# Kernel tuning notes

Measured on AMD Instinct MI355X. Metric: run time of the kernel, lower is better.

## Reference

```python
import jax, jax.numpy as jnp
import numpy as np

N, NF, DIM, H, DH, DEPTH, EDIM, NB = 256, 127, 128, 8, 64, 6, 3, 512
INNER = H * DH  # 512
SCALE = DH ** -0.5
EPS = 1e-5


def setup_inputs() -> dict:
    key = jax.random.key(0)
    ks = jax.random.split(key, 16)
    p = lambda k, shape: jax.random.normal(k, shape, jnp.float32) * 0.02
    return {
        "coordinates": jax.random.normal(ks[0], (N, 3), jnp.float32),
        "bonds": jax.random.randint(ks[1], (NB, 2), 0, N),
        "noise_level": jax.random.uniform(ks[2], (1,), jnp.float32),
        "atom_emb": p(ks[3], (N, NF)),
        "ln1_g": jnp.ones((DEPTH, DIM)), "ln1_b": jnp.zeros((DEPTH, DIM)),
        "Wq": p(ks[4], (DEPTH, DIM, INNER)), "bq": jnp.zeros((DEPTH, INNER)),
        "Wkv": p(ks[5], (DEPTH, DIM, 2 * INNER)), "bkv": jnp.zeros((DEPTH, 2 * INNER)),
        "We": p(ks[6], (DEPTH, EDIM, INNER)), "be": jnp.zeros((DEPTH, INNER)),
        "Wo": p(ks[7], (DEPTH, INNER, DIM)), "bo": jnp.zeros((DEPTH, DIM)),
        "Wg1": p(ks[8], (DEPTH, 3 * DIM)),
        "ln2_g": jnp.ones((DEPTH, DIM)), "ln2_b": jnp.zeros((DEPTH, DIM)),
        "W1": p(ks[9], (DEPTH, DIM, 4 * DIM)), "b1": jnp.zeros((DEPTH, 4 * DIM)),
        "W2": p(ks[10], (DEPTH, 4 * DIM, DIM)), "b2": jnp.zeros((DEPTH, DIM)),
        "Wg2": p(ks[11], (DEPTH, 3 * DIM)),
        "out_w": p(ks[12], (DIM, 1)), "out_b": jnp.zeros((1,)),
    }


def _layernorm(x, g, b):
    m = jnp.mean(x, axis=-1, keepdims=True)
    v = jnp.mean((x - m) ** 2, axis=-1, keepdims=True)
    return (x - m) * jax.lax.rsqrt(v + EPS) * g + b


def _gated_residual(x, res, Wg):
    # Linear(3*dim -> 1, no bias) then sigmoid; mask is all-True so no masking.
    gate = jax.nn.sigmoid(jnp.concatenate([x, res, x - res], axis=-1) @ Wg)[..., None]
    return x * gate + res * (1.0 - gate)


def _forward(coordinates, bonds, noise_level, atom_emb, ln1_g, ln1_b, Wq, bq,
             Wkv, bkv, We, be, Wo, bo, Wg1, ln2_g, ln2_b, W1, b1, W2, b2, Wg2,
             out_w, out_b):
    n = coordinates.shape[0]
    # nodes: [n, NF] atom embeddings (looked up at arange(n)) + noise column -> [n, DIM]
    noise_col = jnp.broadcast_to(noise_level.reshape(1, 1), (n, 1))
    nodes = jnp.concatenate([atom_emb, noise_col], axis=-1)
    # dense edge tensor [n, n, 3]: coordinate differences at bonded pairs, antisymmetric
    bi, bj = bonds[:, 0], bonds[:, 1]
    diff = coordinates[bi] - coordinates[bj]
    edges = jnp.zeros((n, n, EDIM), jnp.float32).at[bi, bj].set(diff).at[bj, bi].set(-diff)

    for l in range(DEPTH):
        # --- edge-biased multi-head attention (PreNorm) ---
        x = _layernorm(nodes, ln1_g[l], ln1_b[l])
        q = (x @ Wq[l] + bq[l]).reshape(n, H, DH).transpose(1, 0, 2)          # [h, i, d]
        kv = x @ Wkv[l] + bkv[l]
        k = kv[:, :INNER].reshape(n, H, DH).transpose(1, 0, 2)                # [h, j, d]
        v = kv[:, INNER:].reshape(n, H, DH).transpose(1, 0, 2)                # [h, j, d]
        e = (edges @ We[l] + be[l]).reshape(n, n, H, DH).transpose(2, 0, 1, 3)  # [h, i, j, d]
        k_ij = k[:, None, :, :] + e                                            # [h, i, j, d]
        v_ij = v[:, None, :, :] + e
        sim = jnp.einsum('hid,hijd->hij', q, k_ij) * SCALE
        attn = jax.nn.softmax(sim, axis=-1)  # mask is all ones -> no-op
        out = jnp.einsum('hij,hijd->hid', attn, v_ij)                          # [h, i, d]
        out = out.transpose(1, 0, 2).reshape(n, INNER) @ Wo[l] + bo[l]         # [n, DIM]
        nodes = _gated_residual(out, nodes, Wg1[l])
        # --- feedforward (PreNorm) + gated residual ---
        y = _layernorm(nodes, ln2_g[l], ln2_b[l])
        y = jax.nn.gelu(y @ W1[l] + b1[l], approximate=False) @ W2[l] + b2[l]
        nodes = _gated_residual(y, nodes, Wg2[l])

    energy = nodes @ out_w + out_b  # [n, 1]
    return energy[None, :, :]       # [1, n, 1]


def reference(coordinates, bonds, noise_level, atom_emb, ln1_g, ln1_b, Wq, bq,
              Wkv, bkv, We, be, Wo, bo, Wg1, ln2_g, ln2_b, W1, b1, W2, b2, Wg2,
              out_w, out_b):
    return _forward(coordinates, bonds, noise_level, atom_emb, ln1_g, ln1_b,
                    Wq, bq, Wkv, bkv, We, be, Wo, bo, Wg1, ln2_g, ln2_b,
                    W1, b1, W2, b2, Wg2, out_w, out_b)
```

## Files before the change

kernel.cpp:

```cpp
#include <hip/hip_runtime.h>

#define NN     256
#define NF     127
#define DIM    128
#define NH     8
#define DH     64
#define INNER  512
#define DEPTH  6
#define NB     512
#define ATTN_SCALE 0.125f
#define LN_EPS 1e-5f

typedef _Float16 f16;
union H8 { uint4 u; f16 h[8]; };

#define FMA4(A_, S_, V_) { A_.x=fmaf(S_,(V_).x,A_.x); A_.y=fmaf(S_,(V_).y,A_.y); \
                           A_.z=fmaf(S_,(V_).z,A_.z); A_.w=fmaf(S_,(V_).w,A_.w); }

__device__ __forceinline__ float wred_sum(float v){
#pragma unroll
  for(int o=32;o;o>>=1) v += __shfl_xor(v,o);
  return v;
}
__device__ __forceinline__ float wred_max(float v){
#pragma unroll
  for(int o=32;o;o>>=1) v = fmaxf(v,__shfl_xor(v,o));
  return v;
}
__device__ __forceinline__ float2 wred_sum2(float a, float b){
#pragma unroll
  for(int o=32;o;o>>=1){ a += __shfl_xor(a,o); b += __shfl_xor(b,o); }
  return make_float2(a,b);
}

__device__ __forceinline__ void ln_wave(float n0, float n1,
                                        const float* g, const float* b, int l,
                                        float& x0, float& x1){
  float2 sv = wred_sum2(n0+n1, n0*n0+n1*n1);
  float m  = sv.x*(1.f/DIM);
  float var = sv.y*(1.f/DIM) - m*m;
  float rs = rsqrtf(var + LN_EPS);
  x0 = (n0-m)*rs*g[l]    + b[l];
  x1 = (n1-m)*rs*g[64+l] + b[64+l];
}

__device__ __forceinline__ void gate_wave(float o0, float o1, float& n0, float& n1,
                                          const float* Wg, int l){
  float gv = o0*Wg[l]    + n0*Wg[DIM+l]    + (o0-n0)*Wg[2*DIM+l]
           + o1*Wg[64+l] + n1*Wg[DIM+64+l] + (o1-n1)*Wg[2*DIM+64+l];
  gv = wred_sum(gv);
  float gate = 1.f/(1.f + expf(-gv));
  n0 = o0*gate + n0*(1.f-gate);
  n1 = o1*gate + n1*(1.f-gate);
}

__device__ __forceinline__ void mvp128_512h(const float* __restrict__ xin,
                                            const f16* __restrict__ W,
                                            float* __restrict__ SC, int t){
  const int cg8 = (t&63)<<3, fg = t>>6, f0 = fg<<4;
  const f16* __restrict__ p = W + f0*INNER + cg8;
  float4 a0 = make_float4(0.f,0.f,0.f,0.f), a1 = a0;
#pragma unroll
  for(int k=0;k<16;k++){
    H8 wv; wv.u = *(const uint4*)(p + k*INNER);
    float x = xin[f0+k];
    a0.x=fmaf(x,(float)wv.h[0],a0.x); a0.y=fmaf(x,(float)wv.h[1],a0.y);
    a0.z=fmaf(x,(float)wv.h[2],a0.z); a0.w=fmaf(x,(float)wv.h[3],a0.w);
    a1.x=fmaf(x,(float)wv.h[4],a1.x); a1.y=fmaf(x,(float)wv.h[5],a1.y);
    a1.z=fmaf(x,(float)wv.h[6],a1.z); a1.w=fmaf(x,(float)wv.h[7],a1.w);
  }
  *(float4*)(SC + fg*INNER + cg8)     = a0;
  *(float4*)(SC + fg*INNER + cg8 + 4) = a1;
}
__device__ __forceinline__ void mvp512_128h(const float* __restrict__ ain,
                                            const f16* __restrict__ W,
                                            float* __restrict__ SC, int t){
  const int cg8 = (t&15)<<3, fg = t>>4, f0 = fg<<4;
  const f16* __restrict__ p = W + f0*DIM + cg8;
  float4 a0 = make_float4(0.f,0.f,0.f,0.f), a1 = a0;
#pragma unroll
  for(int k=0;k<16;k++){
    H8 wv; wv.u = *(const uint4*)(p + k*DIM);
    float x = ain[f0+k];
    a0.x=fmaf(x,(float)wv.h[0],a0.x); a0.y=fmaf(x,(float)wv.h[1],a0.y);
    a0.z=fmaf(x,(float)wv.h[2],a0.z); a0.w=fmaf(x,(float)wv.h[3],a0.w);
    a1.x=fmaf(x,(float)wv.h[4],a1.x); a1.y=fmaf(x,(float)wv.h[5],a1.y);
    a1.z=fmaf(x,(float)wv.h[6],a1.z); a1.w=fmaf(x,(float)wv.h[7],a1.w);
  }
  *(float4*)(SC + fg*DIM + cg8)     = a0;
  *(float4*)(SC + fg*DIM + cg8 + 4) = a1;
}
__device__ __forceinline__ void mvp128_1024(const float* __restrict__ xin,
                                            const float* __restrict__ W,
                                            float* __restrict__ SC, int t){
  const int cg4 = (t&255)<<2, rh = t>>8;
  float4 acc = make_float4(0.f,0.f,0.f,0.f);
#pragma unroll 8
  for(int f=rh*64; f<rh*64+64; f++){
    float4 wv = *(const float4*)(W + f*(2*INNER) + cg4);
    float xv = xin[f];
    FMA4(acc, xv, wv);
  }
  *(float4*)(SC + rh*(2*INNER) + cg4) = acc;
}

__device__ __forceinline__ void qkv_tail(const float* __restrict__ xs, int i,
    const f16* __restrict__ Wqh, const float* __restrict__ bq,
    const float* __restrict__ Wkv, const float* __restrict__ bkv,
    const float* __restrict__ be, float* qgn, float* kTn, float* vgn,
    float* __restrict__ SC, int t){
  mvp128_512h(xs, Wqh, SC,        t);
  mvp128_1024(xs, Wkv, SC + 4096, t);
  __syncthreads();
  {
    float s = bq[t];
#pragma unroll
    for(int fg=0; fg<8; fg++) s += SC[fg*INNER + t];
    qgn[i*INNER + t] = s;
  }
#pragma unroll
  for(int cc=0; cc<2; cc++){
    int c = t + cc*512;
    float sv = bkv[c] + SC[4096 + c] + SC[4096 + 1024 + c];
    if(c < INNER) kTn[c*NN + i]            = sv + be[c];
    else          vgn[i*INNER + c - INNER] = sv + be[c-INNER];
  }
}

__global__ __launch_bounds__(512) void k_prep(
    const float* __restrict__ Wq, const float* __restrict__ Wo,
    const float* __restrict__ W1, const float* __restrict__ W2,
    f16* Wqh, f16* Woh, f16* W1h, f16* W2h)
{
  const int NQ = DEPTH*DIM*INNER;
  const int NTOT = 4*NQ;
  for(int k = blockIdx.x*512 + threadIdx.x; k < NTOT; k += gridDim.x*512){
    float v; f16* dst;
    if(k < NQ)        { v = Wq[k];        dst = Wqh + k; }
    else if(k < 2*NQ) { v = Wo[k-NQ];     dst = Woh + (k-NQ); }
    else if(k < 3*NQ) { v = W1[k-2*NQ];   dst = W1h + (k-2*NQ); }
    else              { v = W2[k-3*NQ];   dst = W2h + (k-3*NQ); }
    *dst = (f16)v;
  }
}

__global__ __launch_bounds__(512) void k_qkv0(const float* atom_emb, const float* noise,
    float* nodes, const float* ln1_g, const float* ln1_b,
    const f16* Wqh, const float* bq, const float* Wkv, const float* bkv, const float* be,
    float* qg, float* kT, float* vg,
    const int* bonds, const float* coords, float* ebg){
  __shared__ __align__(16) float SC[6144];
  __shared__ __align__(16) float xsm[DIM];
  __shared__ __align__(16) float ebs[8*768];
  const int t = threadIdx.x, bid = blockIdx.x;
  if(bid >= NN){
    const int i0 = (bid-NN)<<3;
#pragma unroll
    for(int cc=0; cc<12; cc++) ebs[cc*512 + t] = 0.f;
    __syncthreads();
    {
      const int bi = bonds[2*t], bj = bonds[2*t+1];
      const bool hi = (bi>=i0 && bi<i0+8), hj = (bj>=i0 && bj<i0+8);
      if(hi || hj){
        float dx = coords[3*bi+0] - coords[3*bj+0];
        float dy = coords[3*bi+1] - coords[3*bj+1];
        float dz = coords[3*bi+2] - coords[3*bj+2];
        if(hi){ float* e = ebs + (bi-i0)*768; e[bj]=dx;  e[256+bj]=dy;  e[512+bj]=dz;  }
        if(hj){ float* e = ebs + (bj-i0)*768; e[bi]=-dx; e[256+bi]=-dy; e[512+bi]=-dz; }
      }
    }
    __syncthreads();
#pragma unroll
    for(int cc=0; cc<12; cc++) ebg[(size_t)i0*768 + cc*512 + t] = ebs[cc*512 + t];
    return;
  }
  const int i = bid, w = t>>6, l = t&63;
  float nd0 = (l<NF)?    atom_emb[i*NF + l]      : noise[0];
  float nd1 = (64+l<NF)? atom_emb[i*NF + 64 + l] : noise[0];
  if(w==0){ nodes[i*DIM + l] = nd0; nodes[i*DIM + 64 + l] = nd1; }
  float x0, x1;
  ln_wave(nd0, nd1, ln1_g, ln1_b, l, x0, x1);
  xsm[l] = x0; xsm[64+l] = x1;
  __syncthreads();
  qkv_tail(xsm, i, Wqh, bq, Wkv, bkv, be, qg, kT, vg, SC, t);
}

__global__ __launch_bounds__(512) void k_attn(
    const float* __restrict__ qg, const float* __restrict__ kT,
    const float* __restrict__ vg, const float* __restrict__ ebg,
    const float* __restrict__ We, float* __restrict__ aog,
    const f16* __restrict__ pfA, const f16* __restrict__ pfB,
    const f16* __restrict__ pfC, const f16* __restrict__ pfD,
    const float* __restrict__ pfE, int pf_next)
{
  __shared__ __align__(16) float kTs[64*NN];
  __shared__ __align__(16) float vs[NN*64];
  __shared__ __align__(16) float aW[8][NN];
  __shared__ __align__(16) float qsm[8*DH];
  const int t = threadIdx.x;
  const int h = blockIdx.x >> 5, i0 = (blockIdx.x & 31) << 3;
  const int w = t>>6, l = t&63;
  const int qb = h*DH, j0 = l<<2;

  {
    const float* kbase = kT + qb*NN;
#pragma unroll
    for(int r=0;r<8;r++){
      int idx = r*2048 + (t<<2);
      *(float4*)(kTs + idx) = *(const float4*)(kbase + idx);
    }
    const int jr = t>>4, c4 = (t&15)<<2;
#pragma unroll
    for(int p=0;p<8;p++){
      int j = p*32 + jr;
      *(float4*)(vs + j*64 + c4) = *(const float4*)(vg + j*INNER + qb + c4);
    }
  }
  qsm[w*DH + l] = qg[(i0+w)*INNER + qb + l];

  {
    const int s = blockIdx.x >> 3;
    unsigned keep = 0u;
    if(t < 256){
      keep ^= ((const uint4*)((const char*)pfA + (size_t)s*4096))[t].x;
      keep ^= ((const uint4*)((const char*)pfB + (size_t)s*4096))[t].y;
      keep ^= ((const uint4*)((const char*)pfC + (size_t)s*4096))[t].z;
      if(pf_next)
        keep ^= ((const uint4*)((const char*)pfD + (size_t)s*4096))[t].w;
    }
    if(pf_next){
      keep ^= ((const uint4*)((const char*)pfE + (size_t)s*16384))[t].x;
      keep ^= ((const uint4*)((const char*)pfE + (size_t)s*16384))[512 + t].x;
    }
    asm volatile("" :: "v"(keep));
  }
  __syncthreads();

  float qwe0, qwe1, qwe2;
  {
    float qv = qsm[w*DH + l];
    qwe0 = qv*We[0*INNER + qb + l];
    qwe1 = qv*We[1*INNER + qb + l];
    qwe2 = qv*We[2*INNER + qb + l];
#pragma unroll
    for(int o=32;o;o>>=1){
      qwe0 += __shfl_xor(qwe0,o); qwe1 += __shfl_xor(qwe1,o); qwe2 += __shfl_xor(qwe2,o);
    }
  }
  float s0=0.f,s1=0.f,s2=0.f,s3=0.f;
#pragma unroll 8
  for(int o=0;o<DH;o++){
    float qv = qsm[w*DH + o];
    float4 kk = *(const float4*)(kTs + o*NN + j0);
    s0=fmaf(qv,kk.x,s0); s1=fmaf(qv,kk.y,s1); s2=fmaf(qv,kk.z,s2); s3=fmaf(qv,kk.w,s3);
  }
  const float* __restrict__ e = ebg + (size_t)(i0+w)*768;
  float4 ex = *(const float4*)(e + j0);
  float4 ey = *(const float4*)(e + 256 + j0);
  float4 ez = *(const float4*)(e + 512 + j0);
  s0 = (s0 + qwe0*ex.x + qwe1*ey.x + qwe2*ez.x)*ATTN_SCALE;
  s1 = (s1 + qwe0*ex.y + qwe1*ey.y + qwe2*ez.y)*ATTN_SCALE;
  s2 = (s2 + qwe0*ex.z + qwe1*ey.z + qwe2*ez.z)*ATTN_SCALE;
  s3 = (s3 + qwe0*ex.w + qwe1*ey.w + qwe2*ez.w)*ATTN_SCALE;
  float mx = wred_max(fmaxf(fmaxf(s0,s1),fmaxf(s2,s3)));
  float p0=expf(s0-mx), p1=expf(s1-mx), p2=expf(s2-mx), p3=expf(s3-mx);
  float inv = 1.f / wred_sum(p0+p1+p2+p3);
  float a0=p0*inv, a1=p1*inv, a2=p2*inv, a3=p3*inv;
  *(float4*)(aW[w] + j0) = make_float4(a0,a1,a2,a3);
  float c0 = a0*ex.x + a1*ex.y + a2*ex.z + a3*ex.w;
  float c1 = a0*ey.x + a1*ey.y + a2*ey.z + a3*ey.w;
  float c2 = a0*ez.x + a1*ez.y + a2*ez.z + a3*ez.w;
  c0 = wred_sum(c0); c1 = wred_sum(c1); c2 = wred_sum(c2);
  __builtin_amdgcn_wave_barrier();
  const float* aww = aW[w];
  float acc0 = 0.f, acc1 = 0.f;
#pragma unroll 8
  for(int j=0;j<NN;j+=2){
    acc0 = fmaf(aww[j],   vs[j*64 + l],     acc0);
    acc1 = fmaf(aww[j+1], vs[(j+1)*64 + l], acc1);
  }
  float ov = acc0 + acc1
           + c0*We[0*INNER + qb + l]
           + c1*We[1*INNER + qb + l]
           + c2*We[2*INNER + qb + l];
  aog[(i0+w)*INNER + qb + l] = ov;
}

__global__ __launch_bounds__(512) void k_layer(
    float* nodes, const float* __restrict__ aog,
    float* qg_n, float* kT_n, float* vg_n,
    const f16* __restrict__ Woh, const float* __restrict__ bo,
    const float* __restrict__ Wg1,
    const float* __restrict__ ln2_g, const float* __restrict__ ln2_b,
    const f16* __restrict__ W1h, const float* __restrict__ b1,
    const f16* __restrict__ W2h, const float* __restrict__ b2,
    const float* __restrict__ Wg2,
    const float* __restrict__ ln1_g_n, const float* __restrict__ ln1_b_n,
    const f16* __restrict__ Wqh_n, const float* __restrict__ bq_n,
    const float* __restrict__ Wkv_n, const float* __restrict__ bkv_n,
    const float* __restrict__ be_n,
    const float* __restrict__ out_w, const float* __restrict__ out_b,
    float* eout, int has_next)
{
  __shared__ __align__(16) float SC[6144];
  __shared__ __align__(16) float qs[INNER];
  __shared__ __align__(16) float aos[INNER];
  __shared__ __align__(16) float xsm[DIM];
  const int t = threadIdx.x, i = blockIdx.x;
  const int w = t>>6, l = t&63;

  aos[t] = aog[i*INNER + t];
  float nd0 = nodes[i*DIM + l];
  float nd1 = nodes[i*DIM + 64 + l];
  __syncthreads();

  mvp512_128h(aos, Woh, SC, t);
  __syncthreads();
  {
    float o0 = bo[l], o1 = bo[64+l];
#pragma unroll
    for(int fg=0; fg<32; fg++){ o0 += SC[fg*DIM + l]; o1 += SC[fg*DIM + 64 + l]; }
    gate_wave(o0, o1, nd0, nd1, Wg1, l);
    float x0, x1;
    ln_wave(nd0, nd1, ln2_g, ln2_b, l, x0, x1);
    xsm[l] = x0; xsm[64+l] = x1;
  }
  __syncthreads();

  mvp128_512h(xsm, W1h, SC, t);
  __syncthreads();
  {
    float a = b1[t];
#pragma unroll
    for(int fg=0; fg<8; fg++) a += SC[fg*INNER + t];
    qs[t] = 0.5f*a*(1.f + erff(a*0.70710678118654752440f));
  }
  __syncthreads();
  mvp512_128h(qs, W2h, SC, t);
  __syncthreads();
  {
    float y0 = b2[l], y1 = b2[64+l];
#pragma unroll
    for(int fg=0; fg<32; fg++){ y0 += SC[fg*DIM + l]; y1 += SC[fg*DIM + 64 + l]; }
    gate_wave(y0, y1, nd0, nd1, Wg2, l);
    if(w==0){ nodes[i*DIM + l] = nd0; nodes[i*DIM + 64 + l] = nd1; }
    if(has_next){
      float x0, x1;
      ln_wave(nd0, nd1, ln1_g_n, ln1_b_n, l, x0, x1);
      xsm[l] = x0; xsm[64+l] = x1;
    } else if(w==0){
      float ev = nd0*out_w[l] + nd1*out_w[64+l];
      ev = wred_sum(ev);
      if(l==0) eout[i] = ev + out_b[0];
    }
  }
  if(has_next){
    __syncthreads();
    qkv_tail(xsm, i, Wqh_n, bq_n, Wkv_n, bkv_n, be_n,
             qg_n, kT_n, vg_n, SC, t);
  }
}

extern "C" void kernel_launch(void* const* d_in, const int* in_sizes, int n_in,
                              void* d_out, int out_size, void* d_ws, size_t ws_size,
                              hipStream_t stream){
  const float* coords   = (const float*)d_in[0];
  const int*   bonds    = (const int*  )d_in[1];
  const float* noise    = (const float*)d_in[2];
  const float* atom_emb = (const float*)d_in[3];
  const float* ln1_g = (const float*)d_in[4];
  const float* ln1_b = (const float*)d_in[5];
  const float* Wq    = (const float*)d_in[6];
  const float* bq    = (const float*)d_in[7];
  const float* Wkv   = (const float*)d_in[8];
  const float* bkv   = (const float*)d_in[9];
  const float* We    = (const float*)d_in[10];
  const float* be    = (const float*)d_in[11];
  const float* Wo    = (const float*)d_in[12];
  const float* bo    = (const float*)d_in[13];
  const float* Wg1   = (const float*)d_in[14];
  const float* ln2_g = (const float*)d_in[15];
  const float* ln2_b = (const float*)d_in[16];
  const float* W1    = (const float*)d_in[17];
  const float* b1    = (const float*)d_in[18];
  const float* W2    = (const float*)d_in[19];
  const float* b2    = (const float*)d_in[20];
  const float* Wg2   = (const float*)d_in[21];
  const float* out_w = (const float*)d_in[22];
  const float* out_b = (const float*)d_in[23];

  char* base = (char*)d_ws;
  float* nodes = (float*)(base);
  float* qb0   = (float*)(base + 131072);
  float* qb1   = (float*)(base + 655360);
  float* aog   = (float*)(base + 1179648);
  float* ebg   = (float*)(base + 1703936);
  float* kb0   = (float*)(base + 2490368);
  float* kb1   = (float*)(base + 3014656);
  float* vb0   = (float*)(base + 3538944);
  float* vb1   = (float*)(base + 4063232);
  f16*   Wqh   = (f16*  )(base + 4587520);
  f16*   Woh   = (f16*  )(base + 5373952);
  f16*   W1h   = (f16*  )(base + 6160384);
  f16*   W2h   = (f16*  )(base + 6946816);
  float* eout  = (float*)d_out;

  k_prep<<<512, 512, 0, stream>>>(Wq, Wo, W1, W2, Wqh, Woh, W1h, W2h);
  k_qkv0<<<NN+32, 512, 0, stream>>>(atom_emb, noise, nodes, ln1_g, ln1_b,
                                    Wqh, bq, Wkv, bkv, be,
                                    qb0, kb0, vb0,
                                    bonds, coords, ebg);
  for(int l=0; l<DEPTH; l++){
    int has_next = (l < DEPTH-1);
    int ln = has_next ? l+1 : l;
    float* qcur = (l&1)? qb1:qb0;  float* kcur = (l&1)? kb1:kb0;  float* vcur = (l&1)? vb1:vb0;
    float* qnxt = (l&1)? qb0:qb1;  float* knxt = (l&1)? kb0:kb1;  float* vnxt = (l&1)? vb0:vb1;
    const f16* Woh_l  = Woh + (size_t)l*INNER*DIM;
    const f16* W1h_l  = W1h + (size_t)l*DIM*4*DIM;
    const f16* W2h_l  = W2h + (size_t)l*4*DIM*DIM;
    const f16* Wqh_n  = Wqh + (size_t)ln*DIM*INNER;
    const float* Wkv_n = Wkv + (size_t)ln*DIM*2*INNER;
    k_attn<<<NN, 512, 0, stream>>>(
      qcur, kcur, vcur, ebg,
      We + (size_t)l*3*INNER, aog,
      Woh_l, W1h_l, W2h_l, Wqh_n, Wkv_n, has_next);
    k_layer<<<NN, 512, 0, stream>>>(
      nodes, aog,
      qnxt, knxt, vnxt,
      Woh_l, bo + (size_t)l*DIM, Wg1 + (size_t)l*3*DIM,
      ln2_g + (size_t)l*DIM, ln2_b + (size_t)l*DIM,
      W1h_l, b1 + (size_t)l*4*DIM,
      W2h_l, b2 + (size_t)l*DIM, Wg2 + (size_t)l*3*DIM,
      ln1_g + (size_t)ln*DIM, ln1_b + (size_t)ln*DIM,
      Wqh_n, bq + (size_t)ln*INNER,
      Wkv_n, bkv + (size_t)ln*2*INNER,
      be  + (size_t)ln*INNER,
      out_w, out_b, eout, has_next);
  }
}
```

Measured before the change: 269.8 us.

## Fuse attention and layer kernels with atomic counters; merge prep into init

Attention and the per-node layer MLP now run in one launch of 512 blocks. The layer blocks spin on per-row-group atomic counters until the eight attention blocks producing their rows finish. The f16 weight conversion is merged into the initial QKV kernel, which uses fp32 Wq directly so it does not depend on the conversion. The aim is to cut kernel launches and let layer work start as soon as its attention rows are ready. The cost is spin-wait overhead, a larger shared-memory footprint limiting occupancy, and a deadlock risk if layer blocks are scheduled before attention blocks can run.

```diff
diff --git a/kernel.cpp b/kernel.cpp
--- a/kernel.cpp
+++ b/kernel.cpp
@@ -90,6 +90,19 @@
   *(float4*)(SC + fg*DIM + cg8)     = a0;
   *(float4*)(SC + fg*DIM + cg8 + 4) = a1;
 }
+__device__ __forceinline__ void mvp128_512f(const float* __restrict__ xin,
+                                            const float* __restrict__ W,
+                                            float* __restrict__ SC, int t){
+  const int cg4 = (t&127)<<2, fq = t>>7;
+  float4 acc = make_float4(0.f,0.f,0.f,0.f);
+#pragma unroll 8
+  for(int f=fq*32; f<fq*32+32; f++){
+    float4 wv = *(const float4*)(W + f*INNER + cg4);
+    float xv = xin[f];
+    FMA4(acc, xv, wv);
+  }
+  *(float4*)(SC + fq*INNER + cg4) = acc;
+}
 __device__ __forceinline__ void mvp128_1024(const float* __restrict__ xin,
                                             const float* __restrict__ W,
                                             float* __restrict__ SC, int t){
@@ -127,32 +140,48 @@
   }
 }
 
-__global__ __launch_bounds__(512) void k_prep(
-    const float* __restrict__ Wq, const float* __restrict__ Wo,
-    const float* __restrict__ W1, const float* __restrict__ W2,
-    f16* Wqh, f16* Woh, f16* W1h, f16* W2h)
-{
-  const int NQ = DEPTH*DIM*INNER;
-  const int NTOT = 4*NQ;
-  for(int k = blockIdx.x*512 + threadIdx.x; k < NTOT; k += gridDim.x*512){
-    float v; f16* dst;
-    if(k < NQ)        { v = Wq[k];        dst = Wqh + k; }
-    else if(k < 2*NQ) { v = Wo[k-NQ];     dst = Woh + (k-NQ); }
-    else if(k < 3*NQ) { v = W1[k-2*NQ];   dst = W1h + (k-2*NQ); }
-    else              { v = W2[k-3*NQ];   dst = W2h + (k-3*NQ); }
-    *dst = (f16)v;
-  }
-}
-
-__global__ __launch_bounds__(512) void k_qkv0(const float* atom_emb, const float* noise,
+__device__ __forceinline__ void qkv_tail0f(const float* __restrict__ xs, int i,
+    const float* __restrict__ Wq, const float* __restrict__ bq,
+    const float* __restrict__ Wkv, const float* __restrict__ bkv,
+    const float* __restrict__ be, float* qgn, float* kTn, float* vgn,
+    float* __restrict__ SC, int t){
+  mvp128_512f(xs, Wq,  SC,        t);
+  mvp128_1024(xs, Wkv, SC + 2048, t);
+  __syncthreads();
+  qgn[i*INNER + t] = bq[t] + SC[t] + SC[512+t] + SC[1024+t] + SC[1536+t];
+#pragma unroll
+  for(int cc=0; cc<2; cc++){
+    int c = t + cc*512;
+    float sv = bkv[c] + SC[2048 + c] + SC[2048 + 1024 + c];
+    if(c < INNER) kTn[c*NN + i]            = sv + be[c];
+    else          vgn[i*INNER + c - INNER] = sv + be[c-INNER];
+  }
+}
+
+__global__ __launch_bounds__(512) void k_init(const float* atom_emb, const float* noise,
     float* nodes, const float* ln1_g, const float* ln1_b,
-    const f16* Wqh, const float* bq, const float* Wkv, const float* bkv, const float* be,
+    const float* Wq, const float* bq, const float* Wkv, const float* bkv, const float* be,
     float* qg, float* kT, float* vg,
-    const int* bonds, const float* coords, float* ebg){
+    const int* bonds, const float* coords, float* ebg,
+    const float* Wo, const float* W1, const float* W2,
+    f16* Wqh, f16* Woh, f16* W1h, f16* W2h, int* cnt){
   __shared__ __align__(16) float SC[6144];
   __shared__ __align__(16) float xsm[DIM];
   __shared__ __align__(16) float ebs[8*768];
   const int t = threadIdx.x, bid = blockIdx.x;
+  if(bid >= 288){
+    if(bid == 288 && t < DEPTH*32) cnt[t] = 0;
+    const int NQ = DEPTH*DIM*INNER;
+    for(int k = (bid-288)*512 + t; k < 4*NQ; k += 512*512){
+      float v; f16* dst;
+      if(k < NQ)        { v = Wq[k];        dst = Wqh + k; }
+      else if(k < 2*NQ) { v = Wo[k-NQ];     dst = Woh + (k-NQ); }
+      else if(k < 3*NQ) { v = W1[k-2*NQ];   dst = W1h + (k-2*NQ); }
+      else              { v = W2[k-3*NQ];   dst = W2h + (k-3*NQ); }
+      *dst = (f16)v;
+    }
+    return;
+  }
   if(bid >= NN){
     const int i0 = (bid-NN)<<3;
 #pragma unroll
@@ -182,112 +211,14 @@
   ln_wave(nd0, nd1, ln1_g, ln1_b, l, x0, x1);
   xsm[l] = x0; xsm[64+l] = x1;
   __syncthreads();
-  qkv_tail(xsm, i, Wqh, bq, Wkv, bkv, be, qg, kT, vg, SC, t);
-}
-
-__global__ __launch_bounds__(512) void k_attn(
+  qkv_tail0f(xsm, i, Wq, bq, Wkv, bkv, be, qg, kT, vg, SC, t);
+}
+
+__global__ __launch_bounds__(512) void k_al(
     const float* __restrict__ qg, const float* __restrict__ kT,
     const float* __restrict__ vg, const float* __restrict__ ebg,
     const float* __restrict__ We, float* __restrict__ aog,
-    const f16* __restrict__ pfA, const f16* __restrict__ pfB,
-    const f16* __restrict__ pfC, const f16* __restrict__ pfD,
-    const float* __restrict__ pfE, int pf_next)
-{
-  __shared__ __align__(16) float kTs[64*NN];
-  __shared__ __align__(16) float vs[NN*64];
-  __shared__ __align__(16) float aW[8][NN];
-  __shared__ __align__(16) float qsm[8*DH];
-  const int t = threadIdx.x;
-  const int h = blockIdx.x >> 5, i0 = (blockIdx.x & 31) << 3;
-  const int w = t>>6, l = t&63;
-  const int qb = h*DH, j0 = l<<2;
-
-  {
-    const float* kbase = kT + qb*NN;
-#pragma unroll
-    for(int r=0;r<8;r++){
-      int idx = r*2048 + (t<<2);
-      *(float4*)(kTs + idx) = *(const float4*)(kbase + idx);
-    }
-    const int jr = t>>4, c4 = (t&15)<<2;
-#pragma unroll
-    for(int p=0;p<8;p++){
-      int j = p*32 + jr;
-      *(float4*)(vs + j*64 + c4) = *(const float4*)(vg + j*INNER + qb + c4);
-    }
-  }
-  qsm[w*DH + l] = qg[(i0+w)*INNER + qb + l];
-
-  {
-    const int s = blockIdx.x >> 3;
-    unsigned keep = 0u;
-    if(t < 256){
-      keep ^= ((const uint4*)((const char*)pfA + (size_t)s*4096))[t].x;
-      keep ^= ((const uint4*)((const char*)pfB + (size_t)s*4096))[t].y;
-      keep ^= ((const uint4*)((const char*)pfC + (size_t)s*4096))[t].z;
-      if(pf_next)
-        keep ^= ((const uint4*)((const char*)pfD + (size_t)s*4096))[t].w;
-    }
-    if(pf_next){
-      keep ^= ((const uint4*)((const char*)pfE + (size_t)s*16384))[t].x;
-      keep ^= ((const uint4*)((const char*)pfE + (size_t)s*16384))[512 + t].x;
-    }
-    asm volatile("" :: "v"(keep));
-  }
-  __syncthreads();
-
-  float qwe0, qwe1, qwe2;
-  {
-    float qv = qsm[w*DH + l];
-    qwe0 = qv*We[0*INNER + qb + l];
-    qwe1 = qv*We[1*INNER + qb + l];
-    qwe2 = qv*We[2*INNER + qb + l];
-#pragma unroll
-    for(int o=32;o;o>>=1){
-      qwe0 += __shfl_xor(qwe0,o); qwe1 += __shfl_xor(qwe1,o); qwe2 += __shfl_xor(qwe2,o);
-    }
-  }
-  float s0=0.f,s1=0.f,s2=0.f,s3=0.f;
-#pragma unroll 8
-  for(int o=0;o<DH;o++){
-    float qv = qsm[w*DH + o];
-    float4 kk = *(const float4*)(kTs + o*NN + j0);
-    s0=fmaf(qv,kk.x,s0); s1=fmaf(qv,kk.y,s1); s2=fmaf(qv,kk.z,s2); s3=fmaf(qv,kk.w,s3);
-  }
-  const float* __restrict__ e = ebg + (size_t)(i0+w)*768;
-  float4 ex = *(const float4*)(e + j0);
-  float4 ey = *(const float4*)(e + 256 + j0);
-  float4 ez = *(const float4*)(e + 512 + j0);
-  s0 = (s0 + qwe0*ex.x + qwe1*ey.x + qwe2*ez.x)*ATTN_SCALE;
-  s1 = (s1 + qwe0*ex.y + qwe1*ey.y + qwe2*ez.y)*ATTN_SCALE;
-  s2 = (s2 + qwe0*ex.z + qwe1*ey.z + qwe2*ez.z)*ATTN_SCALE;
-  s3 = (s3 + qwe0*ex.w + qwe1*ey.w + qwe2*ez.w)*ATTN_SCALE;
-  float mx = wred_max(fmaxf(fmaxf(s0,s1),fmaxf(s2,s3)));
-  float p0=expf(s0-mx), p1=expf(s1-mx), p2=expf(s2-mx), p3=expf(s3-mx);
-  float inv = 1.f / wred_sum(p0+p1+p2+p3);
-  float a0=p0*inv, a1=p1*inv, a2=p2*inv, a3=p3*inv;
-  *(float4*)(aW[w] + j0) = make_float4(a0,a1,a2,a3);
-  float c0 = a0*ex.x + a1*ex.y + a2*ex.z + a3*ex.w;
-  float c1 = a0*ey.x + a1*ey.y + a2*ey.z + a3*ey.w;
-  float c2 = a0*ez.x + a1*ez.y + a2*ez.z + a3*ez.w;
-  c0 = wred_sum(c0); c1 = wred_sum(c1); c2 = wred_sum(c2);
-  __builtin_amdgcn_wave_barrier();
-  const float* aww = aW[w];
-  float acc0 = 0.f, acc1 = 0.f;
-#pragma unroll 8
-  for(int j=0;j<NN;j+=2){
-    acc0 = fmaf(aww[j],   vs[j*64 + l],     acc0);
-    acc1 = fmaf(aww[j+1], vs[(j+1)*64 + l], acc1);
-  }
-  float ov = acc0 + acc1
-           + c0*We[0*INNER + qb + l]
-           + c1*We[1*INNER + qb + l]
-           + c2*We[2*INNER + qb + l];
-  aog[(i0+w)*INNER + qb + l] = ov;
-}
-
-__global__ __launch_bounds__(512) void k_layer(
-    float* nodes, const float* __restrict__ aog,
+    float* nodes,
     float* qg_n, float* kT_n, float* vg_n,
     const f16* __restrict__ Woh, const float* __restrict__ bo,
     const float* __restrict__ Wg1,
@@ -300,18 +231,126 @@
     const float* __restrict__ Wkv_n, const float* __restrict__ bkv_n,
     const float* __restrict__ be_n,
     const float* __restrict__ out_w, const float* __restrict__ out_b,
-    float* eout, int has_next)
+    float* eout, int* cnt_l, int has_next)
 {
-  __shared__ __align__(16) float SC[6144];
-  __shared__ __align__(16) float qs[INNER];
-  __shared__ __align__(16) float aos[INNER];
-  __shared__ __align__(16) float xsm[DIM];
-  const int t = threadIdx.x, i = blockIdx.x;
+  __shared__ __align__(16) float smem[35328];
+  const int t = threadIdx.x, bid = blockIdx.x;
+
+  if(bid < NN){
+    float* kTs = smem;
+    float* vs  = smem + 16384;
+    float* aW  = smem + 32768;
+    float* qsm = smem + 34816;
+    const int h = bid >> 5, i0 = (bid & 31) << 3;
+    const int w = t>>6, l = t&63;
+    const int qb = h*DH, j0 = l<<2;
+
+    {
+      const float* kbase = kT + qb*NN;
+#pragma unroll
+      for(int r=0;r<8;r++){
+        int idx = r*2048 + (t<<2);
+        *(float4*)(kTs + idx) = *(const float4*)(kbase + idx);
+      }
+      const int jr = t>>4, c4 = (t&15)<<2;
+#pragma unroll
+      for(int p=0;p<8;p++){
+        int j = p*32 + jr;
+        *(float4*)(vs + j*64 + c4) = *(const float4*)(vg + j*INNER + qb + c4);
+      }
+    }
+    qsm[w*DH + l] = qg[(i0+w)*INNER + qb + l];
+
+    {
+      const int s = bid >> 3;
+      unsigned keep = 0u;
+      if(t < 256){
+        keep ^= ((const uint4*)((const char*)Woh   + (size_t)s*4096))[t].x;
+        keep ^= ((const uint4*)((const char*)W1h   + (size_t)s*4096))[t].y;
+        keep ^= ((const uint4*)((const char*)W2h   + (size_t)s*4096))[t].z;
+        if(has_next)
+          keep ^= ((const uint4*)((const char*)Wqh_n + (size_t)s*4096))[t].w;
+      }
+      if(has_next){
+        keep ^= ((const uint4*)((const char*)Wkv_n + (size_t)s*16384))[t].x;
+        keep ^= ((const uint4*)((const char*)Wkv_n + (size_t)s*16384))[512 + t].x;
+      }
+      asm volatile("" :: "v"(keep));
+    }
+    __syncthreads();
+
+    float qwe0, qwe1, qwe2;
+    {
+      float qv = qsm[w*DH + l];
+      qwe0 = qv*We[0*INNER + qb + l];
+      qwe1 = qv*We[1*INNER + qb + l];
+      qwe2 = qv*We[2*INNER + qb + l];
+#pragma unroll
+      for(int o=32;o;o>>=1){
+        qwe0 += __shfl_xor(qwe0,o); qwe1 += __shfl_xor(qwe1,o); qwe2 += __shfl_xor(qwe2,o);
+      }
+    }
+    float s0=0.f,s1=0.f,s2=0.f,s3=0.f;
+#pragma unroll 8
+    for(int o=0;o<DH;o++){
+      float qv = qsm[w*DH + o];
+      float4 kk = *(const float4*)(kTs + o*NN + j0);
+      s0=fmaf(qv,kk.x,s0); s1=fmaf(qv,kk.y,s1); s2=fmaf(qv,kk.z,s2); s3=fmaf(qv,kk.w,s3);
+    }
+    const float* __restrict__ e = ebg + (size_t)(i0+w)*768;
+    float4 ex = *(const float4*)(e + j0);
+    float4 ey = *(const float4*)(e + 256 + j0);
+    float4 ez = *(const float4*)(e + 512 + j0);
+    s0 = (s0 + qwe0*ex.x + qwe1*ey.x + qwe2*ez.x)*ATTN_SCALE;
+    s1 = (s1 + qwe0*ex.y + qwe1*ey.y + qwe2*ez.y)*ATTN_SCALE;
+    s2 = (s2 + qwe0*ex.z + qwe1*ey.z + qwe2*ez.z)*ATTN_SCALE;
+    s3 = (s3 + qwe0*ex.w + qwe1*ey.w + qwe2*ez.w)*ATTN_SCALE;
+    float mx = wred_max(fmaxf(fmaxf(s0,s1),fmaxf(s2,s3)));
+    float p0=expf(s0-mx), p1=expf(s1-mx), p2=expf(s2-mx), p3=expf(s3-mx);
+    float inv = 1.f / wred_sum(p0+p1+p2+p3);
+    float a0=p0*inv, a1=p1*inv, a2=p2*inv, a3=p3*inv;
+    *(float4*)(aW + w*NN + j0) = make_float4(a0,a1,a2,a3);
+    float c0 = a0*ex.x + a1*ex.y + a2*ex.z + a3*ex.w;
+    float c1 = a0*ey.x + a1*ey.y + a2*ey.z + a3*ey.w;
+    float c2 = a0*ez.x + a1*ez.y + a2*ez.z + a3*ez.w;
+    c0 = wred_sum(c0); c1 = wred_sum(c1); c2 = wred_sum(c2);
+    __builtin_amdgcn_wave_barrier();
+    const float* aww = aW + w*NN;
+    float acc0 = 0.f, acc1 = 0.f;
+#pragma unroll 8
+    for(int j=0;j<NN;j+=2){
+      acc0 = fmaf(aww[j],   vs[j*64 + l],     acc0);
+      acc1 = fmaf(aww[j+1], vs[(j+1)*64 + l], acc1);
+    }
+    float ov = acc0 + acc1
+             + c0*We[0*INNER + qb + l]
+             + c1*We[1*INNER + qb + l]
+             + c2*We[2*INNER + qb + l];
+    aog[(i0+w)*INNER + qb + l] = ov;
+    __syncthreads();
+    if(t==0){
+      __threadfence();
+      atomicAdd(cnt_l + (bid & 31), 1);
+    }
+    return;
+  }
+
+  float* SC  = smem;
+  float* qs  = smem + 6144;
+  float* aos = smem + 6656;
+  float* xsm = smem + 7168;
+  const int i = bid - NN;
   const int w = t>>6, l = t&63;
 
-  aos[t] = aog[i*INNER + t];
   float nd0 = nodes[i*DIM + l];
   float nd1 = nodes[i*DIM + 64 + l];
+
+  if(t==0){
+    while(atomicAdd(cnt_l + (i>>3), 0) < 8){ __builtin_amdgcn_s_sleep(2); }
+    __threadfence();
+  }
+  __syncthreads();
+  aos[t] = aog[i*INNER + t];
   __syncthreads();
 
   mvp512_128h(aos, Woh, SC, t);
@@ -403,13 +442,14 @@
   f16*   Woh   = (f16*  )(base + 5373952);
   f16*   W1h   = (f16*  )(base + 6160384);
   f16*   W2h   = (f16*  )(base + 6946816);
+  int*   cnt   = (int*  )(base + 7733248);
   float* eout  = (float*)d_out;
 
-  k_prep<<<512, 512, 0, stream>>>(Wq, Wo, W1, W2, Wqh, Woh, W1h, W2h);
-  k_qkv0<<<NN+32, 512, 0, stream>>>(atom_emb, noise, nodes, ln1_g, ln1_b,
-                                    Wqh, bq, Wkv, bkv, be,
-                                    qb0, kb0, vb0,
-                                    bonds, coords, ebg);
+  k_init<<<800, 512, 0, stream>>>(atom_emb, noise, nodes, ln1_g, ln1_b,
+                                  Wq, bq, Wkv, bkv, be,
+                                  qb0, kb0, vb0,
+                                  bonds, coords, ebg,
+                                  Wo, W1, W2, Wqh, Woh, W1h, W2h, cnt);
   for(int l=0; l<DEPTH; l++){
     int has_next = (l < DEPTH-1);
     int ln = has_next ? l+1 : l;
@@ -420,12 +460,10 @@
     const f16* W2h_l  = W2h + (size_t)l*4*DIM*DIM;
     const f16* Wqh_n  = Wqh + (size_t)ln*DIM*INNER;
     const float* Wkv_n = Wkv + (size_t)ln*DIM*2*INNER;
-    k_attn<<<NN, 512, 0, stream>>>(
+    k_al<<<2*NN, 512, 0, stream>>>(
       qcur, kcur, vcur, ebg,
       We + (size_t)l*3*INNER, aog,
-      Woh_l, W1h_l, W2h_l, Wqh_n, Wkv_n, has_next);
-    k_layer<<<NN, 512, 0, stream>>>(
-      nodes, aog,
+      nodes,
       qnxt, knxt, vnxt,
       Woh_l, bo + (size_t)l*DIM, Wg1 + (size_t)l*3*DIM,
       ln2_g + (size_t)l*DIM, ln2_b + (size_t)l*DIM,
@@ -435,6 +473,6 @@
       Wqh_n, bq + (size_t)ln*INNER,
       Wkv_n, bkv + (size_t)ln*2*INNER,
       be  + (size_t)ln*INNER,
-      out_w, out_b, eout, has_next);
-  }
-}
+      out_w, out_b, eout, cnt + l*32, has_next);
+  }
+}
```

Result: slower. 317.7 us (+17.7%).

## Split QKV projection into a separate row-tiled kernel reusing weights across rows

Applied to the files above, without the earlier changes.

Moves the per-node Q/K/V projection out of k_layer and k_qkv0 into a new k_qkv kernel. Each block handles 32 rows by 64 output columns, so every weight load is reused across 32 nodes instead of reloaded per node. The Wq fp16 conversion is dropped because Q now reads fp32 weights directly, and the remaining weight conversion is folded into the init kernel. The cost is five extra kernel launches, a round trip of the normalised activations through global memory, and losing the next-layer prefetch in k_attn.

```diff
diff --git a/kernel.cpp b/kernel.cpp
--- a/kernel.cpp
+++ b/kernel.cpp
@@ -90,69 +90,23 @@
   *(float4*)(SC + fg*DIM + cg8)     = a0;
   *(float4*)(SC + fg*DIM + cg8 + 4) = a1;
 }
-__device__ __forceinline__ void mvp128_1024(const float* __restrict__ xin,
-                                            const float* __restrict__ W,
-                                            float* __restrict__ SC, int t){
-  const int cg4 = (t&255)<<2, rh = t>>8;
-  float4 acc = make_float4(0.f,0.f,0.f,0.f);
-#pragma unroll 8
-  for(int f=rh*64; f<rh*64+64; f++){
-    float4 wv = *(const float4*)(W + f*(2*INNER) + cg4);
-    float xv = xin[f];
-    FMA4(acc, xv, wv);
-  }
-  *(float4*)(SC + rh*(2*INNER) + cg4) = acc;
-}
-
-__device__ __forceinline__ void qkv_tail(const float* __restrict__ xs, int i,
-    const f16* __restrict__ Wqh, const float* __restrict__ bq,
-    const float* __restrict__ Wkv, const float* __restrict__ bkv,
-    const float* __restrict__ be, float* qgn, float* kTn, float* vgn,
-    float* __restrict__ SC, int t){
-  mvp128_512h(xs, Wqh, SC,        t);
-  mvp128_1024(xs, Wkv, SC + 4096, t);
-  __syncthreads();
-  {
-    float s = bq[t];
-#pragma unroll
-    for(int fg=0; fg<8; fg++) s += SC[fg*INNER + t];
-    qgn[i*INNER + t] = s;
-  }
-#pragma unroll
-  for(int cc=0; cc<2; cc++){
-    int c = t + cc*512;
-    float sv = bkv[c] + SC[4096 + c] + SC[4096 + 1024 + c];
-    if(c < INNER) kTn[c*NN + i]            = sv + be[c];
-    else          vgn[i*INNER + c - INNER] = sv + be[c-INNER];
-  }
-}
-
-__global__ __launch_bounds__(512) void k_prep(
-    const float* __restrict__ Wq, const float* __restrict__ Wo,
-    const float* __restrict__ W1, const float* __restrict__ W2,
-    f16* Wqh, f16* Woh, f16* W1h, f16* W2h)
-{
-  const int NQ = DEPTH*DIM*INNER;
-  const int NTOT = 4*NQ;
-  for(int k = blockIdx.x*512 + threadIdx.x; k < NTOT; k += gridDim.x*512){
-    float v; f16* dst;
-    if(k < NQ)        { v = Wq[k];        dst = Wqh + k; }
-    else if(k < 2*NQ) { v = Wo[k-NQ];     dst = Woh + (k-NQ); }
-    else if(k < 3*NQ) { v = W1[k-2*NQ];   dst = W1h + (k-2*NQ); }
-    else              { v = W2[k-3*NQ];   dst = W2h + (k-3*NQ); }
-    *dst = (f16)v;
-  }
-}
-
-__global__ __launch_bounds__(512) void k_qkv0(const float* atom_emb, const float* noise,
-    float* nodes, const float* ln1_g, const float* ln1_b,
-    const f16* Wqh, const float* bq, const float* Wkv, const float* bkv, const float* be,
-    float* qg, float* kT, float* vg,
-    const int* bonds, const float* coords, float* ebg){
-  __shared__ __align__(16) float SC[6144];
-  __shared__ __align__(16) float xsm[DIM];
+
+__global__ __launch_bounds__(512) void k_init(const float* atom_emb, const float* noise,
+    float* nodes, const float* ln1_g, const float* ln1_b, float* xg0,
+    const int* bonds, const float* coords, float* ebg,
+    const float* Wo, const float* W1, const float* W2,
+    f16* Woh, f16* W1h, f16* W2h){
   __shared__ __align__(16) float ebs[8*768];
   const int t = threadIdx.x, bid = blockIdx.x;
+  if(bid >= 288){
+    const int NQ = DEPTH*DIM*INNER;
+    for(int k = (bid-288)*512 + t; k < 3*NQ; k += 512*512){
+      if(k < NQ)        W1h[k]      = (f16)W1[k];
+      else if(k < 2*NQ) Woh[k-NQ]   = (f16)Wo[k-NQ];
+      else              W2h[k-2*NQ] = (f16)W2[k-2*NQ];
+    }
+    return;
+  }
   if(bid >= NN){
     const int i0 = (bid-NN)<<3;
 #pragma unroll
@@ -177,12 +131,60 @@
   const int i = bid, w = t>>6, l = t&63;
   float nd0 = (l<NF)?    atom_emb[i*NF + l]      : noise[0];
   float nd1 = (64+l<NF)? atom_emb[i*NF + 64 + l] : noise[0];
-  if(w==0){ nodes[i*DIM + l] = nd0; nodes[i*DIM + 64 + l] = nd1; }
   float x0, x1;
   ln_wave(nd0, nd1, ln1_g, ln1_b, l, x0, x1);
-  xsm[l] = x0; xsm[64+l] = x1;
-  __syncthreads();
-  qkv_tail(xsm, i, Wqh, bq, Wkv, bkv, be, qg, kT, vg, SC, t);
+  if(w==0){
+    nodes[i*DIM + l] = nd0; nodes[i*DIM + 64 + l] = nd1;
+    xg0[i*DIM + l] = x0;    xg0[i*DIM + 64 + l] = x1;
+  }
+}
+
+__global__ __launch_bounds__(512) void k_qkv(
+    const float* __restrict__ xg,
+    const float* __restrict__ Wq, const float* __restrict__ bq,
+    const float* __restrict__ Wkv, const float* __restrict__ bkv,
+    const float* __restrict__ be,
+    float* __restrict__ qg, float* __restrict__ kT, float* __restrict__ vg){
+  __shared__ __align__(16) float xs[32*DIM];
+  const int t = threadIdx.x, bid = blockIdx.x;
+  const int rt = bid / 24, ct = bid % 24;
+  const int cb = ct*64;
+  const int jl = t>>4, j = rt*32 + jl;
+  const int c  = cb + ((t&15)<<2);
+#pragma unroll
+  for(int r=0;r<2;r++){
+    int idx = r*2048 + (t<<2);
+    *(float4*)(xs + idx) = *(const float4*)(xg + (size_t)rt*32*DIM + idx);
+  }
+  __syncthreads();
+  const float* __restrict__ Wp; int stride;
+  if(cb < 512){ Wp = Wq + c;          stride = 512;  }
+  else        { Wp = Wkv + (c - 512); stride = 1024; }
+  float4 acc = make_float4(0.f,0.f,0.f,0.f);
+  const float* xrow = xs + jl*DIM;
+#pragma unroll 16
+  for(int f=0; f<DIM; f++){
+    float4 wv = *(const float4*)(Wp + f*stride);
+    float xv = xrow[f];
+    FMA4(acc, xv, wv);
+  }
+  if(cb < 512){
+    acc.x += bq[c];   acc.y += bq[c+1]; acc.z += bq[c+2]; acc.w += bq[c+3];
+    *(float4*)(qg + j*INNER + c) = acc;
+  } else if(cb < 1024){
+    int kc = c - 512;
+    kT[(kc+0)*NN + j] = acc.x + bkv[kc+0] + be[kc+0];
+    kT[(kc+1)*NN + j] = acc.y + bkv[kc+1] + be[kc+1];
+    kT[(kc+2)*NN + j] = acc.z + bkv[kc+2] + be[kc+2];
+    kT[(kc+3)*NN + j] = acc.w + bkv[kc+3] + be[kc+3];
+  } else {
+    int vc = c - 1024;
+    acc.x += bkv[512+vc+0] + be[vc+0];
+    acc.y += bkv[512+vc+1] + be[vc+1];
+    acc.z += bkv[512+vc+2] + be[vc+2];
+    acc.w += bkv[512+vc+3] + be[vc+3];
+    *(float4*)(vg + j*INNER + vc) = acc;
+  }
 }
 
 __global__ __launch_bounds__(512) void k_attn(
@@ -190,8 +192,7 @@
     const float* __restrict__ vg, const float* __restrict__ ebg,
     const float* __restrict__ We, float* __restrict__ aog,
     const f16* __restrict__ pfA, const f16* __restrict__ pfB,
-    const f16* __restrict__ pfC, const f16* __restrict__ pfD,
-    const float* __restrict__ pfE, int pf_next)
+    const f16* __restrict__ pfC)
 {
   __shared__ __align__(16) float kTs[64*NN];
   __shared__ __align__(16) float vs[NN*64];
@@ -225,12 +226,6 @@
       keep ^= ((const uint4*)((const char*)pfA + (size_t)s*4096))[t].x;
       keep ^= ((const uint4*)((const char*)pfB + (size_t)s*4096))[t].y;
       keep ^= ((const uint4*)((const char*)pfC + (size_t)s*4096))[t].z;
-      if(pf_next)
-        keep ^= ((const uint4*)((const char*)pfD + (size_t)s*4096))[t].w;
-    }
-    if(pf_next){
-      keep ^= ((const uint4*)((const char*)pfE + (size_t)s*16384))[t].x;
-      keep ^= ((const uint4*)((const char*)pfE + (size_t)s*16384))[512 + t].x;
     }
     asm volatile("" :: "v"(keep));
   }
@@ -287,8 +282,7 @@
 }
 
 __global__ __launch_bounds__(512) void k_layer(
-    float* nodes, const float* __restrict__ aog,
-    float* qg_n, float* kT_n, float* vg_n,
+    float* nodes, const float* __restrict__ aog, float* xg_n,
     const f16* __restrict__ Woh, const float* __restrict__ bo,
     const float* __restrict__ Wg1,
     const float* __restrict__ ln2_g, const float* __restrict__ ln2_b,
@@ -296,13 +290,10 @@
     const f16* __restrict__ W2h, const float* __restrict__ b2,
     const float* __restrict__ Wg2,
     const float* __restrict__ ln1_g_n, const float* __restrict__ ln1_b_n,
-    const f16* __restrict__ Wqh_n, const float* __restrict__ bq_n,
-    const float* __restrict__ Wkv_n, const float* __restrict__ bkv_n,
-    const float* __restrict__ be_n,
     const float* __restrict__ out_w, const float* __restrict__ out_b,
     float* eout, int has_next)
 {
-  __shared__ __align__(16) float SC[6144];
+  __shared__ __align__(16) float SC[4096];
   __shared__ __align__(16) float qs[INNER];
   __shared__ __align__(16) float aos[INNER];
   __shared__ __align__(16) float xsm[DIM];
@@ -347,17 +338,12 @@
     if(has_next){
       float x0, x1;
       ln_wave(nd0, nd1, ln1_g_n, ln1_b_n, l, x0, x1);
-      xsm[l] = x0; xsm[64+l] = x1;
+      if(w==0){ xg_n[i*DIM + l] = x0; xg_n[i*DIM + 64 + l] = x1; }
     } else if(w==0){
       float ev = nd0*out_w[l] + nd1*out_w[64+l];
       ev = wred_sum(ev);
       if(l==0) eout[i] = ev + out_b[0];
     }
-  }
-  if(has_next){
-    __syncthreads();
-    qkv_tail(xsm, i, Wqh_n, bq_n, Wkv_n, bkv_n, be_n,
-             qg_n, kT_n, vg_n, SC, t);
   }
 }
 
@@ -391,50 +377,47 @@
 
   char* base = (char*)d_ws;
   float* nodes = (float*)(base);
-  float* qb0   = (float*)(base + 131072);
-  float* qb1   = (float*)(base + 655360);
-  float* aog   = (float*)(base + 1179648);
-  float* ebg   = (float*)(base + 1703936);
-  float* kb0   = (float*)(base + 2490368);
-  float* kb1   = (float*)(base + 3014656);
-  float* vb0   = (float*)(base + 3538944);
-  float* vb1   = (float*)(base + 4063232);
-  f16*   Wqh   = (f16*  )(base + 4587520);
-  f16*   Woh   = (f16*  )(base + 5373952);
-  f16*   W1h   = (f16*  )(base + 6160384);
-  f16*   W2h   = (f16*  )(base + 6946816);
+  float* qb    = (float*)(base + 131072);
+  float* kb    = (float*)(base + 655360);
+  float* vb    = (float*)(base + 1179648);
+  float* aog   = (float*)(base + 1703936);
+  float* ebg   = (float*)(base + 2228224);
+  float* xg0   = (float*)(base + 3014656);
+  float* xg1   = (float*)(base + 3145728);
+  f16*   Woh   = (f16*  )(base + 3276800);
+  f16*   W1h   = (f16*  )(base + 4063232);
+  f16*   W2h   = (f16*  )(base + 4849664);
   float* eout  = (float*)d_out;
 
-  k_prep<<<512, 512, 0, stream>>>(Wq, Wo, W1, W2, Wqh, Woh, W1h, W2h);
-  k_qkv0<<<NN+32, 512, 0, stream>>>(atom_emb, noise, nodes, ln1_g, ln1_b,
-                                    Wqh, bq, Wkv, bkv, be,
-                                    qb0, kb0, vb0,
-                                    bonds, coords, ebg);
+  k_init<<<800, 512, 0, stream>>>(atom_emb, noise, nodes, ln1_g, ln1_b, xg0,
+                                  bonds, coords, ebg,
+                                  Wo, W1, W2, Woh, W1h, W2h);
+  k_qkv<<<192, 512, 0, stream>>>(xg0, Wq, bq, Wkv, bkv, be, qb, kb, vb);
   for(int l=0; l<DEPTH; l++){
     int has_next = (l < DEPTH-1);
     int ln = has_next ? l+1 : l;
-    float* qcur = (l&1)? qb1:qb0;  float* kcur = (l&1)? kb1:kb0;  float* vcur = (l&1)? vb1:vb0;
-    float* qnxt = (l&1)? qb0:qb1;  float* knxt = (l&1)? kb0:kb1;  float* vnxt = (l&1)? vb0:vb1;
+    float* xin_next = ((l+1)&1)? xg1 : xg0;
     const f16* Woh_l  = Woh + (size_t)l*INNER*DIM;
     const f16* W1h_l  = W1h + (size_t)l*DIM*4*DIM;
     const f16* W2h_l  = W2h + (size_t)l*4*DIM*DIM;
-    const f16* Wqh_n  = Wqh + (size_t)ln*DIM*INNER;
-    const float* Wkv_n = Wkv + (size_t)ln*DIM*2*INNER;
     k_attn<<<NN, 512, 0, stream>>>(
-      qcur, kcur, vcur, ebg,
+      qb, kb, vb, ebg,
       We + (size_t)l*3*INNER, aog,
-      Woh_l, W1h_l, W2h_l, Wqh_n, Wkv_n, has_next);
+      Woh_l, W1h_l, W2h_l);
     k_layer<<<NN, 512, 0, stream>>>(
-      nodes, aog,
-      qnxt, knxt, vnxt,
+      nodes, aog, xin_next,
       Woh_l, bo + (size_t)l*DIM, Wg1 + (size_t)l*3*DIM,
       ln2_g + (size_t)l*DIM, ln2_b + (size_t)l*DIM,
       W1h_l, b1 + (size_t)l*4*DIM,
       W2h_l, b2 + (size_t)l*DIM, Wg2 + (size_t)l*3*DIM,
       ln1_g + (size_t)ln*DIM, ln1_b + (size_t)ln*DIM,
-      Wqh_n, bq + (size_t)ln*INNER,
-      Wkv_n, bkv + (size_t)ln*2*INNER,
-      be  + (size_t)ln*INNER,
       out_w, out_b, eout, has_next);
-  }
-}
+    if(has_next){
+      k_qkv<<<192, 512, 0, stream>>>(xin_next,
+        Wq  + (size_t)ln*DIM*INNER,   bq  + (size_t)ln*INNER,
+        Wkv + (size_t)ln*DIM*2*INNER, bkv + (size_t)ln*2*INNER,
+        be  + (size_t)ln*INNER,
+        qb, kb, vb);
+    }
+  }
+}
```

Measured after the change: 422.3 us. +56.5%, slower.
